# Optimization experiments

Hardware: AMD Instinct MI355X
Metric: run time of the kernel (lower is better)

## Reference

```python
import jax, jax.numpy as jnp
import numpy as np

B, S, H, FD, P = 32, 512, 768, 64, 30  # batch, seq, hidden(768 fixed), fusion_dim, proj(30 fixed)


def setup_inputs() -> dict:
    key = jax.random.key(0)
    ks = jax.random.split(key, 6)
    return {
        "hidden_states": jax.random.normal(ks[0], (B, S, H), jnp.float32),
        "audio_data": jax.random.normal(ks[1], (B, S, FD), jnp.float32),
        "attention_mask": jnp.zeros((B, 1, 1, S), jnp.float32),  # BERT extended mask, 0 = attend
        "W_t": jax.random.normal(ks[2], (P, H), jnp.float32) * 0.02,   # Conv1d(768,30,k=1) weight
        "W_a": jax.random.normal(ks[3], (P, FD), jnp.float32) * 0.02,  # Conv1d(fusion_dim,30,k=1) weight
        "text_w": jnp.ones((1,), jnp.float32),
        "audio_w": jnp.ones((1,), jnp.float32),
        "fusion_b": jnp.zeros((1,), jnp.float32),
        "W_dense": jax.random.normal(ks[4], (H, H), jnp.float32) * 0.02,  # Linear(768,768), [out,in]
        "b_dense": jnp.zeros((H,), jnp.float32),
        "ln_w": jnp.ones((H,), jnp.float32),
        "ln_b": jnp.zeros((H,), jnp.float32),
    }


def reference(hidden_states, audio_data, attention_mask, W_t, W_a,
              text_w, audio_w, fusion_b, W_dense, b_dense, ln_w, ln_b):
    # attention_mask.squeeze(1) -> [B,1,S]; permute(0,2,1) -> [B,S,1]
    mask = attention_mask[:, 0]                     # [B,1,S]
    mask_t = jnp.transpose(mask, (0, 2, 1))         # [B,S,1]

    # proj_t: Conv1d k=1 == per-position linear
    text = jnp.einsum('bsh,ph->bsp', hidden_states, W_t)      # [B,S,30]
    # original detaches this normalizer (numpy path)
    norm = jax.lax.stop_gradient(jnp.sqrt(jnp.linalg.norm(text.reshape(-1))))
    text = text / norm

    audio = jnp.einsum('bsf,pf->bsp', audio_data, W_a)        # [B,S,30]

    text_att1 = jax.nn.relu(jnp.einsum('bsp,btp->bst', text, text))    # [B,S,S]
    audio_att = jax.nn.relu(jnp.einsum('bsp,btp->bst', audio, audio))  # [B,S,S]

    fusion_att_raw = text_w * text_att1 + audio_w * audio_att + fusion_b
    fusion_att1 = jax.nn.relu(fusion_att_raw)

    att = jax.nn.softmax(fusion_att_raw + mask + mask_t, axis=-1)      # [B,S,S]
    fusion_data = jnp.einsum('bst,bth->bsh', att, hidden_states) + hidden_states

    h = fusion_data @ W_dense.T + b_dense                              # [B,S,768]
    # BertLayerNorm (TF-style, eps inside sqrt)
    u = h.mean(-1, keepdims=True)
    s = ((h - u) ** 2).mean(-1, keepdims=True)
    h = ln_w * (h - u) / jnp.sqrt(s + 1e-12) + ln_b

    return (h[:, 0], text_att1, fusion_att1)
```

## Files before the change

kernel.cpp:

```cpp
#include <hip/hip_runtime.h>
#include <math.h>

#define BB 32
#define SS 512
#define HH 768
#define FDD 64
#define PP 30

typedef __attribute__((ext_vector_type(8))) short short8v;
typedef __attribute__((ext_vector_type(4))) float f32x4;

#define O_TEXTF  0u
#define O_AUDF   524288u
#define O_ATT    1048576u
#define O_SCORE  1064960u
#define O_FPART  1081344u
#define O_HPART  1277952u
#define O_WDT    1572864u
#define O_WTB    2162688u
#define O_WAB    2174976u
#define O_TEXTB  2176000u
#define O_AUDB   2438144u
#define O_SUMSQ  2700288u

__device__ __forceinline__ unsigned short f2bf(float f){
  unsigned u = __float_as_uint(f);
  unsigned r = (u + 0x7fffu + ((u>>16)&1u)) >> 16;
  return (unsigned short)r;
}
__device__ __forceinline__ float d4(const float4& a, const float4& b){
  return a.x*b.x + a.y*b.y + a.z*b.z + a.w*b.w;
}

__global__ __launch_bounds__(256) void k_prep(const float* __restrict__ Wd,
    const float* __restrict__ Wt, const float* __restrict__ Wa, float* __restrict__ ws){
  const int bi = blockIdx.x, tid = threadIdx.x;
  if (bi < 576){
    __shared__ float L[32][33];
    const int tx = bi % 24, ty = bi / 24;
    const int lx = tid & 31, ly = tid >> 5;
    #pragma unroll
    for (int i = 0; i < 4; ++i)
      L[ly + i*8][lx] = Wd[(size_t)(ty*32 + ly + i*8)*HH + tx*32 + lx];
    __syncthreads();
    #pragma unroll
    for (int i = 0; i < 4; ++i)
      ws[O_WDT + (size_t)(tx*32 + ly + i*8)*HH + ty*32 + lx] = L[lx][ly + i*8];
  } else if (bi < 680){
    int idx = (bi - 576)*256 + tid;
    if (idx < 24576){
      int j = idx & 7, lane = (idx>>3) & 63, t = idx>>9;
      int n = t / 24, ks = t - n*24;
      int p = n*16 + (lane & 15);
      int k = ks*32 + ((lane>>4)<<3) + j;
      float v = (p < PP) ? Wt[p*HH + k] : 0.0f;
      ((unsigned short*)(ws + O_WTB))[idx] = f2bf(v);
    } else {
      int fa = idx - 24576;
      int j = fa & 7, lane = (fa>>3) & 63, t = fa>>9;
      int n = t>>1, ks = t & 1;
      int p = n*16 + (lane & 15);
      int k = ks*32 + ((lane>>4)<<3) + j;
      float v = (p < PP) ? Wa[p*FDD + k] : 0.0f;
      ((unsigned short*)(ws + O_WAB))[fa] = f2bf(v);
    }
  } else if (tid == 0){
    ws[O_SUMSQ] = 0.0f;
  }
}

__global__ __launch_bounds__(256) void k_proj(const float* __restrict__ hs,
    const float* __restrict__ ad, float* __restrict__ ws){
  __shared__ __align__(16) unsigned short Ast[64*32];
  const int tid = threadIdx.x;
  const int lane = tid & 63, w = tid >> 6;
  const int rowbase = blockIdx.x * 64;
  const int tr = tid >> 2, tq = tid & 3;
  const int wrunit = ((tr>>4)<<6) + (tr & 15) + (tq<<4);
  const short8v* WTB = (const short8v*)(ws + O_WTB);
  const short8v* WAB = (const short8v*)(ws + O_WAB);
  f32x4 accT0 = {0,0,0,0}, accT1 = {0,0,0,0};

  const float* hsr = hs + (size_t)(rowbase + tr)*HH + tq*8;
  float4 p0 = *(const float4*)hsr, p1 = *(const float4*)(hsr + 4);
  for (int ks = 0; ks < 24; ++ks){
    __syncthreads();
    uint4 pk;
    pk.x = f2bf(p0.x) | ((unsigned)f2bf(p0.y) << 16);
    pk.y = f2bf(p0.z) | ((unsigned)f2bf(p0.w) << 16);
    pk.z = f2bf(p1.x) | ((unsigned)f2bf(p1.y) << 16);
    pk.w = f2bf(p1.z) | ((unsigned)f2bf(p1.w) << 16);
    *(uint4*)&Ast[wrunit*8] = pk;
    if (ks < 23){ hsr += 32; p0 = *(const float4*)hsr; p1 = *(const float4*)(hsr + 4); }
    __syncthreads();
    short8v a = *(const short8v*)&Ast[(w*64 + lane)*8];
    short8v b0 = WTB[ks*64 + lane];
    short8v b1 = WTB[(24 + ks)*64 + lane];
    accT0 = __builtin_amdgcn_mfma_f32_16x16x32_bf16(a, b0, accT0, 0, 0, 0);
    accT1 = __builtin_amdgcn_mfma_f32_16x16x32_bf16(a, b1, accT1, 0, 0, 0);
  }

  f32x4 accA0 = {0,0,0,0}, accA1 = {0,0,0,0};
  for (int ks = 0; ks < 2; ++ks){
    const float* adr = ad + (size_t)(rowbase + tr)*FDD + ks*32 + tq*8;
    float4 q0 = *(const float4*)adr, q1 = *(const float4*)(adr + 4);
    __syncthreads();
    uint4 pk;
    pk.x = f2bf(q0.x) | ((unsigned)f2bf(q0.y) << 16);
    pk.y = f2bf(q0.z) | ((unsigned)f2bf(q0.w) << 16);
    pk.z = f2bf(q1.x) | ((unsigned)f2bf(q1.y) << 16);
    pk.w = f2bf(q1.z) | ((unsigned)f2bf(q1.w) << 16);
    *(uint4*)&Ast[wrunit*8] = pk;
    __syncthreads();
    short8v a = *(const short8v*)&Ast[(w*64 + lane)*8];
    accA0 = __builtin_amdgcn_mfma_f32_16x16x32_bf16(a, WAB[ks*64 + lane], accA0, 0, 0, 0);
    accA1 = __builtin_amdgcn_mfma_f32_16x16x32_bf16(a, WAB[(2 + ks)*64 + lane], accA1, 0, 0, 0);
  }

  float* TEXTF = ws + O_TEXTF;
  float* AUDF  = ws + O_AUDF;
  unsigned short* TEXTB = (unsigned short*)(ws + O_TEXTB);
  unsigned short* AUDB  = (unsigned short*)(ws + O_AUDB);
  const int q4 = lane >> 4, pl = lane & 15;
  float sq = 0.0f;
  #pragma unroll
  for (int r = 0; r < 4; ++r){
    int row = rowbase + w*16 + q4*4 + r;
    float v0 = accT0[r], v1 = accT1[r];
    sq += v0*v0 + v1*v1;
    TEXTF[(size_t)row*32 + pl]      = v0;
    TEXTF[(size_t)row*32 + 16 + pl] = v1;
    TEXTB[(size_t)row*32 + pl]      = f2bf(v0);
    TEXTB[(size_t)row*32 + 16 + pl] = f2bf(v1);
    float a0 = accA0[r], a1 = accA1[r];
    AUDF[(size_t)row*32 + pl]      = a0;
    AUDF[(size_t)row*32 + 16 + pl] = a1;
    AUDB[(size_t)row*32 + pl]      = f2bf(a0);
    AUDB[(size_t)row*32 + 16 + pl] = f2bf(a1);
  }
  #pragma unroll
  for (int off = 32; off; off >>= 1) sq += __shfl_xor(sq, off);
  if (lane == 0) atomicAdd(ws + O_SUMSQ, sq);
}

__global__ __launch_bounds__(256) void k_gram(const float* __restrict__ ws,
    const float* __restrict__ twp, const float* __restrict__ awp, const float* __restrict__ fbp,
    float* __restrict__ out_text, float* __restrict__ out_fus){
  const int tid = threadIdx.x, lane = tid & 63, w = tid >> 6;
  const int tt = blockIdx.x, st = blockIdx.y, b = blockIdx.z;
  const unsigned short* TEXTB = (const unsigned short*)(ws + O_TEXTB);
  const unsigned short* AUDB  = (const unsigned short*)(ws + O_AUDB);
  const int q4 = lane >> 4, pl = lane & 15;
  const size_t srow  = (size_t)b*SS + st*64 + w*16 + pl;
  const size_t trow0 = (size_t)b*SS + tt*64 + pl;
  short8v at = *(const short8v*)&TEXTB[srow*32 + q4*8];
  short8v aa = *(const short8v*)&AUDB [srow*32 + q4*8];
  f32x4 z = {0,0,0,0};
  f32x4 ct[4], ca[4];
  #pragma unroll
  for (int n = 0; n < 4; ++n){
    short8v bt = *(const short8v*)&TEXTB[(trow0 + n*16)*32 + q4*8];
    short8v ba = *(const short8v*)&AUDB [(trow0 + n*16)*32 + q4*8];
    ct[n] = __builtin_amdgcn_mfma_f32_16x16x32_bf16(at, bt, z, 0, 0, 0);
    ca[n] = __builtin_amdgcn_mfma_f32_16x16x32_bf16(aa, ba, z, 0, 0, 0);
  }
  const float inv_s = 1.0f / sqrtf(ws[O_SUMSQ]);
  const float tw = twp[0], aw = awp[0], fb = fbp[0];
  #pragma unroll
  for (int n = 0; n < 4; ++n){
    #pragma unroll
    for (int r = 0; r < 4; ++r){
      float t_ = fmaxf(ct[n][r]*inv_s, 0.0f);
      float a_ = fmaxf(ca[n][r], 0.0f);
      float f_ = fmaxf(tw*t_ + aw*a_ + fb, 0.0f);
      int sr = st*64 + w*16 + q4*4 + r;
      int tc = tt*64 + n*16 + pl;
      size_t o = ((size_t)b*SS + sr)*SS + tc;
      out_text[o] = t_;
      out_fus[o]  = f_;
    }
  }
}

__global__ __launch_bounds__(256) void k_score(float* __restrict__ ws, const float* __restrict__ amask,
    const float* __restrict__ twp, const float* __restrict__ awp, const float* __restrict__ fbp){
  const int b = blockIdx.y, tid = threadIdx.x;
  const int t = blockIdx.x*256 + tid;
  __shared__ __align__(16) float t0[32], a0[32];
  const float* TEXTF = ws + O_TEXTF;
  const float* AUDF  = ws + O_AUDF;
  if (tid < 32){
    t0[tid] = TEXTF[(size_t)b*SS*32 + tid];
    a0[tid] = AUDF [(size_t)b*SS*32 + tid];
  }
  __syncthreads();
  const float inv_s = 1.0f / sqrtf(ws[O_SUMSQ]);
  const float tw = twp[0], aw = awp[0], fb = fbp[0];
  const float m0 = amask[(size_t)b*SS];
  const float4* t04 = (const float4*)t0;
  const float4* a04 = (const float4*)a0;
  const float4* tr = (const float4*)(TEXTF + ((size_t)b*SS + t)*32);
  const float4* ar = (const float4*)(AUDF  + ((size_t)b*SS + t)*32);
  float dt = 0.f, da = 0.f;
  #pragma unroll
  for (int q = 0; q < 8; ++q){ dt += d4(t04[q], tr[q]); da += d4(a04[q], ar[q]); }
  ws[O_SCORE + (size_t)b*SS + t] =
      tw*fmaxf(dt*inv_s, 0.f) + aw*fmaxf(da, 0.f) + fb + amask[(size_t)b*SS + t] + m0;
}

__global__ __launch_bounds__(512) void k_soft(float* __restrict__ ws){
  const int b = blockIdx.x, tid = threadIdx.x;
  __shared__ float red[512];
  const float sv = ws[O_SCORE + (size_t)b*SS + tid];
  red[tid] = sv;
  __syncthreads();
  for (int s2 = 256; s2 > 0; s2 >>= 1){ if (tid < s2) red[tid] = fmaxf(red[tid], red[tid+s2]); __syncthreads(); }
  const float m = red[0];
  __syncthreads();
  const float e = __expf(sv - m);
  red[tid] = e;
  __syncthreads();
  for (int s2 = 256; s2 > 0; s2 >>= 1){ if (tid < s2) red[tid] += red[tid+s2]; __syncthreads(); }
  ws[O_ATT + (size_t)b*SS + tid] = e / red[0];
}

__global__ __launch_bounds__(256) void k_pv(const float* __restrict__ hs, float* __restrict__ ws){
  const int tid = threadIdx.x;
  const int cx = blockIdx.x, th = blockIdx.y, b = blockIdx.z;
  __shared__ float a[64];
  if (tid < 64) a[tid] = ws[O_ATT + (size_t)b*SS + th*64 + tid];
  __syncthreads();
  const int c = cx*256 + tid;
  const float* hp = hs + ((size_t)b*SS + th*64)*HH + c;
  float acc = 0.f;
  #pragma unroll 8
  for (int t = 0; t < 64; ++t) acc += a[t]*hp[(size_t)t*HH];
  if (th == 0) acc += hs[(size_t)b*SS*HH + c];
  ws[O_FPART + ((size_t)th*BB + b)*HH + c] = acc;
}

__global__ __launch_bounds__(256) void k_dense(float* __restrict__ ws){
  const int kc = blockIdx.x, b = blockIdx.y, tid = threadIdx.x;
  __shared__ float fc[64];
  if (tid < 64){
    float s = 0.f;
    const int c = kc*64 + tid;
    #pragma unroll
    for (int th = 0; th < 8; ++th) s += ws[O_FPART + ((size_t)th*BB + b)*HH + c];
    fc[tid] = s;
  }
  __syncthreads();
  const float* Wp = ws + O_WDT + (size_t)(kc*64)*HH;
  float a0 = 0.f, a1 = 0.f, a2 = 0.f;
  #pragma unroll 8
  for (int i = 0; i < 64; ++i){
    const float fv = fc[i];
    const float* wr = Wp + (size_t)i*HH + tid;
    a0 += fv*wr[0];
    a1 += fv*wr[256];
    a2 += fv*wr[512];
  }
  float* hp = ws + O_HPART + ((size_t)kc*BB + b)*HH;
  hp[tid]       = a0;
  hp[tid + 256] = a1;
  hp[tid + 512] = a2;
}

__global__ __launch_bounds__(256) void k_ln(const float* __restrict__ ws,
    const float* __restrict__ bd, const float* __restrict__ lw, const float* __restrict__ lb,
    float* __restrict__ out){
  const int b = blockIdx.x, tid = threadIdx.x;
  __shared__ float red[256];
  float a0 = bd[tid], a1 = bd[tid+256], a2 = bd[tid+512];
  #pragma unroll
  for (int kc = 0; kc < 12; ++kc){
    const float* hp = ws + O_HPART + ((size_t)kc*BB + b)*HH;
    a0 += hp[tid];
    a1 += hp[tid + 256];
    a2 += hp[tid + 512];
  }
  red[tid] = a0 + a1 + a2;
  __syncthreads();
  for (int s2 = 128; s2 > 0; s2 >>= 1){ if (tid < s2) red[tid] += red[tid+s2]; __syncthreads(); }
  const float u = red[0]*(1.0f/HH);
  __syncthreads();
  const float d0 = a0-u, d1 = a1-u, d2 = a2-u;
  red[tid] = d0*d0 + d1*d1 + d2*d2;
  __syncthreads();
  for (int s2 = 128; s2 > 0; s2 >>= 1){ if (tid < s2) red[tid] += red[tid+s2]; __syncthreads(); }
  const float isd = 1.0f / sqrtf(red[0]*(1.0f/HH) + 1e-12f);
  out[(size_t)b*HH + tid]     = lw[tid]    *d0*isd + lb[tid];
  out[(size_t)b*HH + tid+256] = lw[tid+256]*d1*isd + lb[tid+256];
  out[(size_t)b*HH + tid+512] = lw[tid+512]*d2*isd + lb[tid+512];
}

extern "C" void kernel_launch(void* const* d_in, const int* in_sizes, int n_in,
                              void* d_out, int out_size, void* d_ws, size_t ws_size,
                              hipStream_t stream){
  const float* hs    = (const float*)d_in[0];
  const float* ad    = (const float*)d_in[1];
  const float* amask = (const float*)d_in[2];
  const float* Wt    = (const float*)d_in[3];
  const float* Wa    = (const float*)d_in[4];
  const float* twp   = (const float*)d_in[5];
  const float* awp   = (const float*)d_in[6];
  const float* fbp   = (const float*)d_in[7];
  const float* Wd    = (const float*)d_in[8];
  const float* bd    = (const float*)d_in[9];
  const float* lw    = (const float*)d_in[10];
  const float* lb    = (const float*)d_in[11];
  float* out = (float*)d_out;
  float* ws  = (float*)d_ws;
  float* out_h    = out;
  float* out_text = out + (size_t)BB*HH;
  float* out_fus  = out_text + (size_t)BB*SS*SS;

  hipLaunchKernelGGL(k_prep, dim3(681), dim3(256), 0, stream, Wd, Wt, Wa, ws);
  hipLaunchKernelGGL(k_proj, dim3(BB*SS/64), dim3(256), 0, stream, hs, ad, ws);
  hipLaunchKernelGGL(k_gram, dim3(8,8,BB), dim3(256), 0, stream, ws, twp, awp, fbp, out_text, out_fus);
  hipLaunchKernelGGL(k_score, dim3(2,BB), dim3(256), 0, stream, ws, amask, twp, awp, fbp);
  hipLaunchKernelGGL(k_soft, dim3(BB), dim3(512), 0, stream, ws);
  hipLaunchKernelGGL(k_pv, dim3(3,8,BB), dim3(256), 0, stream, hs, ws);
  hipLaunchKernelGGL(k_dense, dim3(12,BB), dim3(256), 0, stream, ws);
  hipLaunchKernelGGL(k_ln, dim3(BB), dim3(256), 0, stream, ws, bd, lw, lb, out_h);
}
```

Measured before the change: 179.4 us.

## Fuse score+softmax and dense+LN, drop LDS staging in proj, vectorize gram stores

Several changes at once. k_proj loads hidden rows straight into MFMA operand registers, removing the LDS staging and barriers, and writes the fp32 projections transposed (feature-major) so row-0 scoring reads are coalesced. k_gram swaps MFMA operands so each lane holds four consecutive columns, allowing float4 stores of the two large outputs. k_score and k_soft become one kernel, and k_dense and k_ln become one 1024-thread kernel per batch, cutting two launches and the workspace round trips. The fused dense kernel runs only 32 blocks, which risks lower parallelism for the dense GEMV.

```diff
diff --git a/kernel.cpp b/kernel.cpp
--- a/kernel.cpp
+++ b/kernel.cpp
@@ -6,6 +6,7 @@
 #define HH 768
 #define FDD 64
 #define PP 30
+#define NR 16384
 
 typedef __attribute__((ext_vector_type(8))) short short8v;
 typedef __attribute__((ext_vector_type(4))) float f32x4;
@@ -13,9 +14,7 @@
 #define O_TEXTF  0u
 #define O_AUDF   524288u
 #define O_ATT    1048576u
-#define O_SCORE  1064960u
 #define O_FPART  1081344u
-#define O_HPART  1277952u
 #define O_WDT    1572864u
 #define O_WTB    2162688u
 #define O_WAB    2174976u
@@ -28,8 +27,13 @@
   unsigned r = (u + 0x7fffu + ((u>>16)&1u)) >> 16;
   return (unsigned short)r;
 }
-__device__ __forceinline__ float d4(const float4& a, const float4& b){
-  return a.x*b.x + a.y*b.y + a.z*b.z + a.w*b.w;
+__device__ __forceinline__ short8v pack8(const float4& p0, const float4& p1){
+  union { short8v v; unsigned u[4]; } r;
+  r.u[0] = f2bf(p0.x) | ((unsigned)f2bf(p0.y) << 16);
+  r.u[1] = f2bf(p0.z) | ((unsigned)f2bf(p0.w) << 16);
+  r.u[2] = f2bf(p1.x) | ((unsigned)f2bf(p1.y) << 16);
+  r.u[3] = f2bf(p1.z) | ((unsigned)f2bf(p1.w) << 16);
+  return r.v;
 }
 
 __global__ __launch_bounds__(256) void k_prep(const float* __restrict__ Wd,
@@ -71,72 +75,56 @@
 
 __global__ __launch_bounds__(256) void k_proj(const float* __restrict__ hs,
     const float* __restrict__ ad, float* __restrict__ ws){
-  __shared__ __align__(16) unsigned short Ast[64*32];
   const int tid = threadIdx.x;
   const int lane = tid & 63, w = tid >> 6;
   const int rowbase = blockIdx.x * 64;
-  const int tr = tid >> 2, tq = tid & 3;
-  const int wrunit = ((tr>>4)<<6) + (tr & 15) + (tq<<4);
+  const int mrow = rowbase + w*16 + (lane & 15);
+  const int koff = (lane >> 4) << 3;
   const short8v* WTB = (const short8v*)(ws + O_WTB);
   const short8v* WAB = (const short8v*)(ws + O_WAB);
   f32x4 accT0 = {0,0,0,0}, accT1 = {0,0,0,0};
 
-  const float* hsr = hs + (size_t)(rowbase + tr)*HH + tq*8;
-  float4 p0 = *(const float4*)hsr, p1 = *(const float4*)(hsr + 4);
+  const float* hp = hs + (size_t)mrow*HH + koff;
+  #pragma unroll 4
   for (int ks = 0; ks < 24; ++ks){
-    __syncthreads();
-    uint4 pk;
-    pk.x = f2bf(p0.x) | ((unsigned)f2bf(p0.y) << 16);
-    pk.y = f2bf(p0.z) | ((unsigned)f2bf(p0.w) << 16);
-    pk.z = f2bf(p1.x) | ((unsigned)f2bf(p1.y) << 16);
-    pk.w = f2bf(p1.z) | ((unsigned)f2bf(p1.w) << 16);
-    *(uint4*)&Ast[wrunit*8] = pk;
-    if (ks < 23){ hsr += 32; p0 = *(const float4*)hsr; p1 = *(const float4*)(hsr + 4); }
-    __syncthreads();
-    short8v a = *(const short8v*)&Ast[(w*64 + lane)*8];
-    short8v b0 = WTB[ks*64 + lane];
-    short8v b1 = WTB[(24 + ks)*64 + lane];
-    accT0 = __builtin_amdgcn_mfma_f32_16x16x32_bf16(a, b0, accT0, 0, 0, 0);
-    accT1 = __builtin_amdgcn_mfma_f32_16x16x32_bf16(a, b1, accT1, 0, 0, 0);
+    float4 p0 = *(const float4*)(hp + ks*32);
+    float4 p1 = *(const float4*)(hp + ks*32 + 4);
+    short8v a = pack8(p0, p1);
+    accT0 = __builtin_amdgcn_mfma_f32_16x16x32_bf16(a, WTB[ks*64 + lane], accT0, 0, 0, 0);
+    accT1 = __builtin_amdgcn_mfma_f32_16x16x32_bf16(a, WTB[(24 + ks)*64 + lane], accT1, 0, 0, 0);
   }
 
   f32x4 accA0 = {0,0,0,0}, accA1 = {0,0,0,0};
+  const float* ap = ad + (size_t)mrow*FDD + koff;
+  #pragma unroll
   for (int ks = 0; ks < 2; ++ks){
-    const float* adr = ad + (size_t)(rowbase + tr)*FDD + ks*32 + tq*8;
-    float4 q0 = *(const float4*)adr, q1 = *(const float4*)(adr + 4);
-    __syncthreads();
-    uint4 pk;
-    pk.x = f2bf(q0.x) | ((unsigned)f2bf(q0.y) << 16);
-    pk.y = f2bf(q0.z) | ((unsigned)f2bf(q0.w) << 16);
-    pk.z = f2bf(q1.x) | ((unsigned)f2bf(q1.y) << 16);
-    pk.w = f2bf(q1.z) | ((unsigned)f2bf(q1.w) << 16);
-    *(uint4*)&Ast[wrunit*8] = pk;
-    __syncthreads();
-    short8v a = *(const short8v*)&Ast[(w*64 + lane)*8];
+    float4 q0 = *(const float4*)(ap + ks*32);
+    float4 q1 = *(const float4*)(ap + ks*32 + 4);
+    short8v a = pack8(q0, q1);
     accA0 = __builtin_amdgcn_mfma_f32_16x16x32_bf16(a, WAB[ks*64 + lane], accA0, 0, 0, 0);
     accA1 = __builtin_amdgcn_mfma_f32_16x16x32_bf16(a, WAB[(2 + ks)*64 + lane], accA1, 0, 0, 0);
   }
 
-  float* TEXTF = ws + O_TEXTF;
-  float* AUDF  = ws + O_AUDF;
+  float* TF = ws + O_TEXTF;
+  float* AF = ws + O_AUDF;
   unsigned short* TEXTB = (unsigned short*)(ws + O_TEXTB);
   unsigned short* AUDB  = (unsigned short*)(ws + O_AUDB);
   const int q4 = lane >> 4, pl = lane & 15;
+  const int row0 = rowbase + w*16 + q4*4;
   float sq = 0.0f;
   #pragma unroll
+  for (int r = 0; r < 4; ++r) sq += accT0[r]*accT0[r] + accT1[r]*accT1[r];
+  *(float4*)(TF + (size_t)pl*NR + row0)      = *(float4*)&accT0;
+  *(float4*)(TF + (size_t)(pl+16)*NR + row0) = *(float4*)&accT1;
+  *(float4*)(AF + (size_t)pl*NR + row0)      = *(float4*)&accA0;
+  *(float4*)(AF + (size_t)(pl+16)*NR + row0) = *(float4*)&accA1;
+  #pragma unroll
   for (int r = 0; r < 4; ++r){
-    int row = rowbase + w*16 + q4*4 + r;
-    float v0 = accT0[r], v1 = accT1[r];
-    sq += v0*v0 + v1*v1;
-    TEXTF[(size_t)row*32 + pl]      = v0;
-    TEXTF[(size_t)row*32 + 16 + pl] = v1;
-    TEXTB[(size_t)row*32 + pl]      = f2bf(v0);
-    TEXTB[(size_t)row*32 + 16 + pl] = f2bf(v1);
-    float a0 = accA0[r], a1 = accA1[r];
-    AUDF[(size_t)row*32 + pl]      = a0;
-    AUDF[(size_t)row*32 + 16 + pl] = a1;
-    AUDB[(size_t)row*32 + pl]      = f2bf(a0);
-    AUDB[(size_t)row*32 + 16 + pl] = f2bf(a1);
+    int row = row0 + r;
+    TEXTB[(size_t)row*32 + pl]      = f2bf(accT0[r]);
+    TEXTB[(size_t)row*32 + 16 + pl] = f2bf(accT1[r]);
+    AUDB[(size_t)row*32 + pl]       = f2bf(accA0[r]);
+    AUDB[(size_t)row*32 + 16 + pl]  = f2bf(accA1[r]);
   }
   #pragma unroll
   for (int off = 32; off; off >>= 1) sq += __shfl_xor(sq, off);
@@ -161,57 +149,52 @@
   for (int n = 0; n < 4; ++n){
     short8v bt = *(const short8v*)&TEXTB[(trow0 + n*16)*32 + q4*8];
     short8v ba = *(const short8v*)&AUDB [(trow0 + n*16)*32 + q4*8];
-    ct[n] = __builtin_amdgcn_mfma_f32_16x16x32_bf16(at, bt, z, 0, 0, 0);
-    ca[n] = __builtin_amdgcn_mfma_f32_16x16x32_bf16(aa, ba, z, 0, 0, 0);
+    ct[n] = __builtin_amdgcn_mfma_f32_16x16x32_bf16(bt, at, z, 0, 0, 0);
+    ca[n] = __builtin_amdgcn_mfma_f32_16x16x32_bf16(ba, aa, z, 0, 0, 0);
   }
   const float inv_s = 1.0f / sqrtf(ws[O_SUMSQ]);
   const float tw = twp[0], aw = awp[0], fb = fbp[0];
+  const int s = st*64 + w*16 + pl;
+  const int tbase = tt*64;
   #pragma unroll
   for (int n = 0; n < 4; ++n){
+    float4 vt, vf;
+    float* pt_ = (float*)&vt; float* pf_ = (float*)&vf;
     #pragma unroll
     for (int r = 0; r < 4; ++r){
       float t_ = fmaxf(ct[n][r]*inv_s, 0.0f);
       float a_ = fmaxf(ca[n][r], 0.0f);
-      float f_ = fmaxf(tw*t_ + aw*a_ + fb, 0.0f);
-      int sr = st*64 + w*16 + q4*4 + r;
-      int tc = tt*64 + n*16 + pl;
-      size_t o = ((size_t)b*SS + sr)*SS + tc;
-      out_text[o] = t_;
-      out_fus[o]  = f_;
+      pt_[r] = t_;
+      pf_[r] = fmaxf(tw*t_ + aw*a_ + fb, 0.0f);
     }
-  }
-}
-
-__global__ __launch_bounds__(256) void k_score(float* __restrict__ ws, const float* __restrict__ amask,
+    size_t o = ((size_t)b*SS + s)*SS + tbase + n*16 + q4*4;
+    *(float4*)(out_text + o) = vt;
+    *(float4*)(out_fus  + o) = vf;
+  }
+}
+
+__global__ __launch_bounds__(512) void k_att(float* __restrict__ ws, const float* __restrict__ amask,
     const float* __restrict__ twp, const float* __restrict__ awp, const float* __restrict__ fbp){
-  const int b = blockIdx.y, tid = threadIdx.x;
-  const int t = blockIdx.x*256 + tid;
-  __shared__ __align__(16) float t0[32], a0[32];
-  const float* TEXTF = ws + O_TEXTF;
-  const float* AUDF  = ws + O_AUDF;
-  if (tid < 32){
-    t0[tid] = TEXTF[(size_t)b*SS*32 + tid];
-    a0[tid] = AUDF [(size_t)b*SS*32 + tid];
-  }
+  const int b = blockIdx.x, tid = threadIdx.x;
+  __shared__ float t0[32], a0[32];
+  __shared__ float red[512];
+  const float* TF = ws + O_TEXTF;
+  const float* AF = ws + O_AUDF;
+  if (tid < 32) t0[tid] = TF[(size_t)tid*NR + (size_t)b*SS];
+  else if (tid < 64) a0[tid-32] = AF[(size_t)(tid-32)*NR + (size_t)b*SS];
   __syncthreads();
   const float inv_s = 1.0f / sqrtf(ws[O_SUMSQ]);
   const float tw = twp[0], aw = awp[0], fb = fbp[0];
   const float m0 = amask[(size_t)b*SS];
-  const float4* t04 = (const float4*)t0;
-  const float4* a04 = (const float4*)a0;
-  const float4* tr = (const float4*)(TEXTF + ((size_t)b*SS + t)*32);
-  const float4* ar = (const float4*)(AUDF  + ((size_t)b*SS + t)*32);
+  const size_t base = (size_t)b*SS + tid;
   float dt = 0.f, da = 0.f;
   #pragma unroll
-  for (int q = 0; q < 8; ++q){ dt += d4(t04[q], tr[q]); da += d4(a04[q], ar[q]); }
-  ws[O_SCORE + (size_t)b*SS + t] =
-      tw*fmaxf(dt*inv_s, 0.f) + aw*fmaxf(da, 0.f) + fb + amask[(size_t)b*SS + t] + m0;
-}
-
-__global__ __launch_bounds__(512) void k_soft(float* __restrict__ ws){
-  const int b = blockIdx.x, tid = threadIdx.x;
-  __shared__ float red[512];
-  const float sv = ws[O_SCORE + (size_t)b*SS + tid];
+  for (int p = 0; p < 32; ++p){
+    dt += t0[p]*TF[(size_t)p*NR + base];
+    da += a0[p]*AF[(size_t)p*NR + base];
+  }
+  const float sv = tw*fmaxf(dt*inv_s, 0.f) + aw*fmaxf(da, 0.f) + fb
+                 + amask[base] + m0;
   red[tid] = sv;
   __syncthreads();
   for (int s2 = 256; s2 > 0; s2 >>= 1){ if (tid < s2) red[tid] = fmaxf(red[tid], red[tid+s2]); __syncthreads(); }
@@ -221,7 +204,7 @@
   red[tid] = e;
   __syncthreads();
   for (int s2 = 256; s2 > 0; s2 >>= 1){ if (tid < s2) red[tid] += red[tid+s2]; __syncthreads(); }
-  ws[O_ATT + (size_t)b*SS + tid] = e / red[0];
+  ws[O_ATT + base] = e / red[0];
 }
 
 __global__ __launch_bounds__(256) void k_pv(const float* __restrict__ hs, float* __restrict__ ws){
@@ -239,59 +222,51 @@
   ws[O_FPART + ((size_t)th*BB + b)*HH + c] = acc;
 }
 
-__global__ __launch_bounds__(256) void k_dense(float* __restrict__ ws){
-  const int kc = blockIdx.x, b = blockIdx.y, tid = threadIdx.x;
-  __shared__ float fc[64];
-  if (tid < 64){
+__global__ __launch_bounds__(1024) void k_dense_ln(const float* __restrict__ ws,
+    const float* __restrict__ bd, const float* __restrict__ lw, const float* __restrict__ lb,
+    float* __restrict__ out){
+  const int b = blockIdx.x, tid = threadIdx.x;
+  __shared__ float f[HH];
+  __shared__ float part[4*HH];
+  __shared__ float red[1024];
+  if (tid < HH){
     float s = 0.f;
-    const int c = kc*64 + tid;
-    #pragma unroll
-    for (int th = 0; th < 8; ++th) s += ws[O_FPART + ((size_t)th*BB + b)*HH + c];
-    fc[tid] = s;
-  }
-  __syncthreads();
-  const float* Wp = ws + O_WDT + (size_t)(kc*64)*HH;
+    #pragma unroll
+    for (int th = 0; th < 8; ++th) s += ws[O_FPART + ((size_t)th*BB + b)*HH + tid];
+    f[tid] = s;
+  }
+  __syncthreads();
+  const int cc = tid >> 8, o = tid & 255;
+  const float* Wp = ws + O_WDT + (size_t)(cc*192)*HH;
+  const float* fp = f + cc*192;
   float a0 = 0.f, a1 = 0.f, a2 = 0.f;
   #pragma unroll 8
-  for (int i = 0; i < 64; ++i){
-    const float fv = fc[i];
-    const float* wr = Wp + (size_t)i*HH + tid;
+  for (int i = 0; i < 192; ++i){
+    const float fv = fp[i];
+    const float* wr = Wp + (size_t)i*HH + o;
     a0 += fv*wr[0];
     a1 += fv*wr[256];
     a2 += fv*wr[512];
   }
-  float* hp = ws + O_HPART + ((size_t)kc*BB + b)*HH;
-  hp[tid]       = a0;
-  hp[tid + 256] = a1;
-  hp[tid + 512] = a2;
-}
-
-__global__ __launch_bounds__(256) void k_ln(const float* __restrict__ ws,
-    const float* __restrict__ bd, const float* __restrict__ lw, const float* __restrict__ lb,
-    float* __restrict__ out){
-  const int b = blockIdx.x, tid = threadIdx.x;
-  __shared__ float red[256];
-  float a0 = bd[tid], a1 = bd[tid+256], a2 = bd[tid+512];
-  #pragma unroll
-  for (int kc = 0; kc < 12; ++kc){
-    const float* hp = ws + O_HPART + ((size_t)kc*BB + b)*HH;
-    a0 += hp[tid];
-    a1 += hp[tid + 256];
-    a2 += hp[tid + 512];
-  }
-  red[tid] = a0 + a1 + a2;
-  __syncthreads();
-  for (int s2 = 128; s2 > 0; s2 >>= 1){ if (tid < s2) red[tid] += red[tid+s2]; __syncthreads(); }
+  part[cc*HH + o]       = a0;
+  part[cc*HH + o + 256] = a1;
+  part[cc*HH + o + 512] = a2;
+  __syncthreads();
+  float h = 0.f;
+  if (tid < HH)
+    h = part[tid] + part[HH + tid] + part[2*HH + tid] + part[3*HH + tid] + bd[tid];
+  red[tid] = (tid < HH) ? h : 0.f;
+  __syncthreads();
+  for (int s2 = 512; s2 > 0; s2 >>= 1){ if (tid < s2) red[tid] += red[tid+s2]; __syncthreads(); }
   const float u = red[0]*(1.0f/HH);
   __syncthreads();
-  const float d0 = a0-u, d1 = a1-u, d2 = a2-u;
-  red[tid] = d0*d0 + d1*d1 + d2*d2;
-  __syncthreads();
-  for (int s2 = 128; s2 > 0; s2 >>= 1){ if (tid < s2) red[tid] += red[tid+s2]; __syncthreads(); }
+  const float d = h - u;
+  red[tid] = (tid < HH) ? d*d : 0.f;
+  __syncthreads();
+  for (int s2 = 512; s2 > 0; s2 >>= 1){ if (tid < s2) red[tid] += red[tid+s2]; __syncthreads(); }
   const float isd = 1.0f / sqrtf(red[0]*(1.0f/HH) + 1e-12f);
-  out[(size_t)b*HH + tid]     = lw[tid]    *d0*isd + lb[tid];
-  out[(size_t)b*HH + tid+256] = lw[tid+256]*d1*isd + lb[tid+256];
-  out[(size_t)b*HH + tid+512] = lw[tid+512]*d2*isd + lb[tid+512];
+  if (tid < HH)
+    out[(size_t)b*HH + tid] = lw[tid]*d*isd + lb[tid];
 }
 
 extern "C" void kernel_launch(void* const* d_in, const int* in_sizes, int n_in,
@@ -316,11 +291,9 @@
   float* out_fus  = out_text + (size_t)BB*SS*SS;
 
   hipLaunchKernelGGL(k_prep, dim3(681), dim3(256), 0, stream, Wd, Wt, Wa, ws);
-  hipLaunchKernelGGL(k_proj, dim3(BB*SS/64), dim3(256), 0, stream, hs, ad, ws);
+  hipLaunchKernelGGL(k_proj, dim3(NR/64), dim3(256), 0, stream, hs, ad, ws);
   hipLaunchKernelGGL(k_gram, dim3(8,8,BB), dim3(256), 0, stream, ws, twp, awp, fbp, out_text, out_fus);
-  hipLaunchKernelGGL(k_score, dim3(2,BB), dim3(256), 0, stream, ws, amask, twp, awp, fbp);
-  hipLaunchKernelGGL(k_soft, dim3(BB), dim3(512), 0, stream, ws);
+  hipLaunchKernelGGL(k_att, dim3(BB), dim3(512), 0, stream, ws, amask, twp, awp, fbp);
   hipLaunchKernelGGL(k_pv, dim3(3,8,BB), dim3(256), 0, stream, hs, ws);
-  hipLaunchKernelGGL(k_dense, dim3(12,BB), dim3(256), 0, stream, ws);
-  hipLaunchKernelGGL(k_ln, dim3(BB), dim3(256), 0, stream, ws, bd, lw, lb, out_h);
-}
+  hipLaunchKernelGGL(k_dense_ln, dim3(BB), dim3(1024), 0, stream, ws, bd, lw, lb, out_h);
+}
```

Result: slower. 186.8 us (+4.2%).
